# Kernel tuning notes

Hardware: AMD Instinct MI355X
Metric: run time of the kernel (lower is better)

The kernel has to match this reference:

```python
import jax, jax.numpy as jnp
import numpy as np

HIDDEN = 256
HEADS = 1
HEAD_DIM = HIDDEN // HEADS  # internal_dim == hidden (downsample_rate=1)
SQ = 4096        # 64x64 current-frame tokens
N_MEM = 4        # memory frames
N_OBJ = 64       # object-pointer tokens excluded from RoPE
SK = N_MEM * SQ + N_OBJ  # 16448


def _rotate_pairwise(x):
    # [x0, x1, x2, x3, ...] -> [-x1, x0, -x3, x2, ...]
    s = x.shape
    x = x.reshape(s[:-1] + (s[-1] // 2, 2))
    return jnp.stack([-x[..., 1], x[..., 0]], axis=-1).reshape(s)


def setup_inputs() -> dict:
    key = jax.random.key(0)
    ks = jax.random.split(key, 16)
    d = {}
    d["query"] = jax.random.normal(ks[0], (1, 1, SQ, HIDDEN), jnp.float32)
    d["key"] = jax.random.normal(ks[1], (1, 1, SK, HIDDEN), jnp.float32)
    d["value"] = jax.random.normal(ks[2], (1, 1, SK, HIDDEN), jnp.float32)
    # rotary tables broadcast over (B*P, heads) like in the keras code
    d["cos"] = jax.random.uniform(ks[3], (1, 1, SQ, HEAD_DIM), jnp.float32, -1.0, 1.0)
    d["sin"] = jax.random.uniform(ks[4], (1, 1, SQ, HEAD_DIM), jnp.float32, -1.0, 1.0)
    w = 0.02
    d["q_w"] = jax.random.normal(ks[5], (HIDDEN, HIDDEN), jnp.float32) * w
    d["q_b"] = jnp.zeros((HIDDEN,), jnp.float32)
    d["k_w"] = jax.random.normal(ks[6], (HIDDEN, HIDDEN), jnp.float32) * w
    d["k_b"] = jnp.zeros((HIDDEN,), jnp.float32)
    d["v_w"] = jax.random.normal(ks[7], (HIDDEN, HIDDEN), jnp.float32) * w
    d["v_b"] = jnp.zeros((HIDDEN,), jnp.float32)
    d["o_w"] = jax.random.normal(ks[8], (HIDDEN, HIDDEN), jnp.float32) * w
    d["o_b"] = jnp.zeros((HIDDEN,), jnp.float32)
    d["num_k_exclude_rope"] = N_OBJ
    return d


def reference(query, key, value, cos, sin, q_w, q_b, k_w, k_b, v_w, v_b, o_w, o_b, num_k_exclude_rope):
    B, P, Sq, _ = query.shape
    Sk = key.shape[2]
    nex = int(num_k_exclude_rope)

    def heads(x):  # (B,P,S,internal) -> (B*P, H, S, hd)
        s = x.shape
        return x.reshape(s[0] * s[1], s[2], HEADS, HEAD_DIM).transpose(0, 2, 1, 3)

    q = heads(query @ q_w + q_b)
    k = heads(key @ k_w + k_b)
    v = heads(value @ v_w + v_b)

    # 2D rotary embedding (fp32 math, as in the original)
    qf = q.astype(jnp.float32)
    q_emb = (qf * cos + _rotate_pairwise(qf) * sin).astype(q.dtype)

    k_rot = k[:, :, :Sk - nex, :]
    k_pass = k[:, :, Sk - nex:, :] if nex > 0 else None
    if k_rot.shape[2] != Sq:  # rope_k_repeat=True path
        rf = k_rot.shape[2] // Sq
        cos_k = jnp.repeat(cos, rf, axis=2)
        sin_k = jnp.repeat(sin, rf, axis=2)
    else:
        cos_k, sin_k = cos, sin
    kf = k_rot.astype(jnp.float32)
    k_emb = (kf * cos_k + _rotate_pairwise(kf) * sin_k).astype(k.dtype)
    if k_pass is not None:
        k_emb = jnp.concatenate([k_emb, k_pass], axis=2)

    scaling = HEAD_DIM ** -0.5
    scores = jnp.einsum('bhqd,bhkd->bhqk', q_emb, k_emb) * scaling
    attn = jax.nn.softmax(scores, axis=-1)
    out = jnp.einsum('bhqk,bhkd->bhqd', attn, v)  # (B*P, H, Sq, hd)
    out = out.transpose(0, 2, 1, 3).reshape(B, P, Sq, HEADS * HEAD_DIM)
    return out @ o_w + o_b
```

## Files before the change

kernel.cpp:

```cpp
#include <hip/hip_runtime.h>
#include <stdint.h>

typedef _Float16 half_t;
typedef __attribute__((ext_vector_type(8))) _Float16 f16x8;
typedef __attribute__((ext_vector_type(4))) _Float16 f16x4;
typedef __attribute__((ext_vector_type(4))) float f32x4;

#define SQN 4096
#define SKN 16448
#define NROPE 16384
#define NSPLIT 8
#define NTILES 514
#define TPC 65


__global__ __launch_bounds__(256) void wt_kernel(const float* __restrict__ qw,
    const float* __restrict__ kw, const float* __restrict__ vw, const float* __restrict__ ow,
    half_t* __restrict__ wt)
{
    __shared__ float tile[64][65];
    int b = blockIdx.x;
    int mat = b >> 4, t4 = b & 15;
    int k0 = (t4 >> 2) << 6, n0 = (t4 & 3) << 6;
    const float* W = (mat == 0) ? qw : (mat == 1) ? kw : (mat == 2) ? vw : ow;
    half_t* WT = wt + mat * 65536;
    int t = threadIdx.x;
#pragma unroll
    for (int j = 0; j < 16; ++j) {
        int e = j * 256 + t;
        tile[e >> 6][e & 63] = W[(k0 + (e >> 6)) * 256 + n0 + (e & 63)];
    }
    __syncthreads();
#pragma unroll
    for (int j = 0; j < 16; ++j) {
        int e = j * 256 + t;
        WT[(n0 + (e >> 6)) * 256 + k0 + (e & 63)] = (half_t)tile[e & 63][e >> 6];
    }
}

__global__ __launch_bounds__(256) void proj_kernel(
    const float* __restrict__ query, const float* __restrict__ key, const float* __restrict__ value,
    const float* __restrict__ cosp, const float* __restrict__ sinp,
    const half_t* __restrict__ wt,
    const float* __restrict__ qb, const float* __restrict__ kb, const float* __restrict__ vb,
    half_t* __restrict__ Qe, half_t* __restrict__ Ke, half_t* __restrict__ VT)
{
    __shared__ __align__(16) half_t Ws[256 * 40];
    int b = blockIdx.x;
    int mode; long row0;
    const float* X; const half_t* W; const float* bias;
    if (b < 64)       { mode = 0; row0 = (long)b * 64;         X = query; W = wt;           bias = qb; }
    else if (b < 321) { mode = 1; row0 = (long)(b - 64) * 64;  X = key;   W = wt + 65536;   bias = kb; }
    else              { mode = 2; row0 = (long)(b - 321) * 64; X = value; W = wt + 131072;  bias = vb; }

    int tid = threadIdx.x;
    int w = tid >> 6, l = tid & 63;
    int l16 = l & 15, l4 = l >> 4;
    long rw0 = row0 + w * 16;

    f32x4 acc[16];
#pragma unroll
    for (int i = 0; i < 16; ++i) acc[i] = (f32x4){0.f, 0.f, 0.f, 0.f};

    for (int ks = 0; ks < 8; ++ks) {
        __syncthreads();
        {
            const f16x8* src = reinterpret_cast<const f16x8*>(W + tid * 256 + ks * 32);
            f16x8* dst = reinterpret_cast<f16x8*>(Ws + tid * 40);
            dst[0] = src[0]; dst[1] = src[1]; dst[2] = src[2]; dst[3] = src[3];
        }
        __syncthreads();
        const float* xp = X + (rw0 + l16) * 256 + ks * 32 + l4 * 8;
        f32x4 xa = *reinterpret_cast<const f32x4*>(xp);
        f32x4 xb = *reinterpret_cast<const f32x4*>(xp + 4);
        f16x8 af;
#pragma unroll
        for (int j = 0; j < 4; ++j) { af[j] = (half_t)xa[j]; af[4 + j] = (half_t)xb[j]; }
#pragma unroll
        for (int nt = 0; nt < 16; ++nt) {
            f16x8 bf = *reinterpret_cast<const f16x8*>(Ws + (nt * 16 + l16) * 40 + l4 * 8);
            acc[nt] = __builtin_amdgcn_mfma_f32_16x16x32_f16(af, bf, acc[nt], 0, 0, 0);
        }
    }

    bool dorope = (mode == 0) || (mode == 1 && row0 < NROPE);
#pragma unroll
    for (int nt = 0; nt < 16; ++nt) {
        int d = nt * 16 + l16;
        float bv = bias[d];
        f32x4 v = acc[nt];
#pragma unroll
        for (int r = 0; r < 4; ++r) v[r] += bv;
        if (dorope) {
#pragma unroll
            for (int r = 0; r < 4; ++r) {
                long m = rw0 + l4 * 4 + r;
                long crow = (mode == 0) ? m : (m >> 2);
                float c = cosp[crow * 256 + d];
                float s = sinp[crow * 256 + d];
                float val = v[r];
                float other = __shfl_xor(val, 1);
                float rot = (d & 1) ? other : -other;
                v[r] = val * c + rot * s;
            }
        }
        if (mode == 2) {
            f16x4 pk;
#pragma unroll
            for (int r = 0; r < 4; ++r) pk[r] = (half_t)v[r];
            *reinterpret_cast<f16x4*>(VT + (long)d * SKN + rw0 + l4 * 4) = pk;
        } else {
            half_t* O = (mode == 0) ? Qe : Ke;
#pragma unroll
            for (int r = 0; r < 4; ++r)
                O[(rw0 + l4 * 4 + r) * 256 + d] = (half_t)v[r];
        }
    }
}

__global__ __launch_bounds__(512) void flash_kernel(
    const half_t* __restrict__ Qe, const half_t* __restrict__ Ke, const half_t* __restrict__ VT,
    float* __restrict__ Op, float* __restrict__ Mp, float* __restrict__ Lp)
{
    __shared__ __align__(16) half_t Ks[32 * 264];
    __shared__ __align__(16) half_t Vs[256 * 40];
    __shared__ __align__(16) half_t Ps[8][16 * 40];

    int b = blockIdx.x;
    int qb = b & 31;
    int chunk = b >> 5;
    int tid = threadIdx.x;
    int w = tid >> 6, l = tid & 63;
    int l16 = l & 15, l4 = l >> 4;
    long qw0 = (long)qb * 128 + w * 16;

    f16x8 qf[8];
#pragma unroll
    for (int ks = 0; ks < 8; ++ks)
        qf[ks] = *reinterpret_cast<const f16x8*>(Qe + (qw0 + l16) * 256 + ks * 32 + l4 * 8);

    f32x4 o[16];
#pragma unroll
    for (int i = 0; i < 16; ++i) o[i] = (f32x4){0.f, 0.f, 0.f, 0.f};
    float mrun = -3.0e38f;
    float lsum = 0.0f;

    int t0 = chunk * TPC;
    int t1 = t0 + TPC; if (t1 > NTILES) t1 = NTILES;
    const float SC = 0.090168441360f;
    half_t* Pw = Ps[w];

    for (int t = t0; t < t1; ++t) {
        long kv0 = (long)t * 32;
        __syncthreads();
        {
            int r = tid >> 4, seg = tid & 15;
            const f16x8* src = reinterpret_cast<const f16x8*>(Ke + (kv0 + r) * 256 + seg * 16);
            f16x8* dst = reinterpret_cast<f16x8*>(Ks + r * 264 + seg * 16);
            dst[0] = src[0]; dst[1] = src[1];
        }
        {
            int d = tid >> 1, seg = tid & 1;
            const f16x8* src = reinterpret_cast<const f16x8*>(VT + (long)d * SKN + kv0 + seg * 16);
            f16x8* dst = reinterpret_cast<f16x8*>(Vs + d * 40 + seg * 16);
            dst[0] = src[0]; dst[1] = src[1];
        }
        __syncthreads();

        f32x4 s0 = (f32x4){0.f, 0.f, 0.f, 0.f};
        f32x4 s1 = (f32x4){0.f, 0.f, 0.f, 0.f};
#pragma unroll
        for (int ks = 0; ks < 8; ++ks) {
            f16x8 ka0 = *reinterpret_cast<const f16x8*>(Ks + l16 * 264 + ks * 32 + l4 * 8);
            f16x8 ka1 = *reinterpret_cast<const f16x8*>(Ks + (16 + l16) * 264 + ks * 32 + l4 * 8);
            s0 = __builtin_amdgcn_mfma_f32_16x16x32_f16(ka0, qf[ks], s0, 0, 0, 0);
            s1 = __builtin_amdgcn_mfma_f32_16x16x32_f16(ka1, qf[ks], s1, 0, 0, 0);
        }

        float tv[8];
#pragma unroll
        for (int r = 0; r < 4; ++r) { tv[r] = s0[r] * SC; tv[4 + r] = s1[r] * SC; }
        float pm = tv[0];
#pragma unroll
        for (int i = 1; i < 8; ++i) pm = fmaxf(pm, tv[i]);
        pm = fmaxf(pm, __shfl_xor(pm, 16));
        pm = fmaxf(pm, __shfl_xor(pm, 32));

        if (!__all(pm - mrun <= 8.0f)) {
            float mn = fmaxf(mrun, pm);
            float alpha = __builtin_amdgcn_exp2f(mrun - mn);
            lsum *= alpha;
            float ao[4];
#pragma unroll
            for (int r = 0; r < 4; ++r) ao[r] = __shfl(alpha, l4 * 4 + r);
#pragma unroll
            for (int i = 0; i < 16; ++i)
#pragma unroll
                for (int r = 0; r < 4; ++r) o[i][r] *= ao[r];
            mrun = mn;
        }

        float p[8];
        float psum = 0.f;
#pragma unroll
        for (int i = 0; i < 8; ++i) { p[i] = __builtin_amdgcn_exp2f(tv[i] - mrun); psum += p[i]; }
        psum += __shfl_xor(psum, 16);
        psum += __shfl_xor(psum, 32);
        lsum += psum;

        f16x4 pk0, pk1;
#pragma unroll
        for (int r = 0; r < 4; ++r) { pk0[r] = (half_t)p[r]; pk1[r] = (half_t)p[4 + r]; }
        *reinterpret_cast<f16x4*>(Pw + l16 * 40 + l4 * 4) = pk0;
        *reinterpret_cast<f16x4*>(Pw + l16 * 40 + 16 + l4 * 4) = pk1;

        f16x8 pa = *reinterpret_cast<const f16x8*>(Pw + l16 * 40 + l4 * 8);
#pragma unroll
        for (int nt = 0; nt < 16; ++nt) {
            f16x8 vbf = *reinterpret_cast<const f16x8*>(Vs + (nt * 16 + l16) * 40 + l4 * 8);
            o[nt] = __builtin_amdgcn_mfma_f32_16x16x32_f16(pa, vbf, o[nt], 0, 0, 0);
        }
    }

    float* Ob = Op + ((long)chunk * SQN + qw0) * 256;
#pragma unroll
    for (int nt = 0; nt < 16; ++nt)
#pragma unroll
        for (int r = 0; r < 4; ++r)
            Ob[(l4 * 4 + r) * 256 + nt * 16 + l16] = o[nt][r];
    if (l < 16) {
        Mp[(long)chunk * SQN + qw0 + l16] = mrun;
        Lp[(long)chunk * SQN + qw0 + l16] = lsum;
    }
}

__global__ __launch_bounds__(256) void reduce_kernel(
    const float* __restrict__ Op, const float* __restrict__ Mp, const float* __restrict__ Lp,
    half_t* __restrict__ AO)
{
    int tid = threadIdx.x;
    long q = (long)blockIdx.x * 4 + (tid >> 6);
    int d0 = (tid & 63) * 4;
    float mi[NSPLIT];
    float mstar = -3.0e38f;
#pragma unroll
    for (int i = 0; i < NSPLIT; ++i) { mi[i] = Mp[i * SQN + q]; mstar = fmaxf(mstar, mi[i]); }
    f32x4 acc = (f32x4){0.f, 0.f, 0.f, 0.f};
    float lsum = 0.f;
#pragma unroll
    for (int i = 0; i < NSPLIT; ++i) {
        float wgt = __builtin_amdgcn_exp2f(mi[i] - mstar);
        lsum += wgt * Lp[i * SQN + q];
        f32x4 ov = *reinterpret_cast<const f32x4*>(Op + ((long)i * SQN + q) * 256 + d0);
#pragma unroll
        for (int r = 0; r < 4; ++r) acc[r] += wgt * ov[r];
    }
    float inv = 1.0f / lsum;
    f16x4 pk;
#pragma unroll
    for (int r = 0; r < 4; ++r) pk[r] = (half_t)(acc[r] * inv);
    *reinterpret_cast<f16x4*>(AO + q * 256 + d0) = pk;
}

__global__ __launch_bounds__(256) void oproj_kernel(
    const half_t* __restrict__ AO, const half_t* __restrict__ WTo,
    const float* __restrict__ ob, float* __restrict__ out)
{
    int b = blockIdx.x;
    int tid = threadIdx.x;
    int w = tid >> 6, l = tid & 63;
    int l16 = l & 15, l4 = l >> 4;
    long r0 = (long)b * 64 + w * 16;
    f32x4 acc[16];
#pragma unroll
    for (int i = 0; i < 16; ++i) acc[i] = (f32x4){0.f, 0.f, 0.f, 0.f};
#pragma unroll
    for (int ks = 0; ks < 8; ++ks) {
        f16x8 af = *reinterpret_cast<const f16x8*>(AO + (r0 + l16) * 256 + ks * 32 + l4 * 8);
#pragma unroll
        for (int nt = 0; nt < 16; ++nt) {
            f16x8 bf = *reinterpret_cast<const f16x8*>(WTo + (nt * 16 + l16) * 256 + ks * 32 + l4 * 8);
            acc[nt] = __builtin_amdgcn_mfma_f32_16x16x32_f16(af, bf, acc[nt], 0, 0, 0);
        }
    }
#pragma unroll
    for (int nt = 0; nt < 16; ++nt) {
        int d = nt * 16 + l16;
        float bv = ob[d];
#pragma unroll
        for (int r = 0; r < 4; ++r)
            out[(r0 + l4 * 4 + r) * 256 + d] = acc[nt][r] + bv;
    }
}

extern "C" void kernel_launch(void* const* d_in, const int* in_sizes, int n_in,
                              void* d_out, int out_size, void* d_ws, size_t ws_size,
                              hipStream_t stream) {
    const float* query = (const float*)d_in[0];
    const float* key   = (const float*)d_in[1];
    const float* value = (const float*)d_in[2];
    const float* cosp  = (const float*)d_in[3];
    const float* sinp  = (const float*)d_in[4];
    const float* qw = (const float*)d_in[5];
    const float* qb = (const float*)d_in[6];
    const float* kw = (const float*)d_in[7];
    const float* kb = (const float*)d_in[8];
    const float* vw = (const float*)d_in[9];
    const float* vb = (const float*)d_in[10];
    const float* ow = (const float*)d_in[11];
    const float* ob = (const float*)d_in[12];

    char* ws = (char*)d_ws;
    half_t* Qe = (half_t*)(ws);
    half_t* Ke = (half_t*)(ws + 2097152);
    half_t* VT = (half_t*)(ws + 10518528);
    half_t* WT = (half_t*)(ws + 18939904);
    float*  Op = (float*)(ws + 19464192);
    float*  Mp = (float*)(ws + 53018624);
    float*  Lp = (float*)(ws + 53149696);
    half_t* AO = (half_t*)(ws + 53280768);

    hipLaunchKernelGGL(wt_kernel, dim3(64), dim3(256), 0, stream, qw, kw, vw, ow, WT);
    hipLaunchKernelGGL(proj_kernel, dim3(578), dim3(256), 0, stream,
                       query, key, value, cosp, sinp, WT, qb, kb, vb, Qe, Ke, VT);
    hipLaunchKernelGGL(flash_kernel, dim3(256), dim3(512), 0, stream, Qe, Ke, VT, Op, Mp, Lp);
    hipLaunchKernelGGL(reduce_kernel, dim3(1024), dim3(256), 0, stream, Op, Mp, Lp, AO);
    hipLaunchKernelGGL(oproj_kernel, dim3(64), dim3(256), 0, stream, AO, WT + 3 * 65536, ob, (float*)d_out);
}
```

Before: 216.6 us.

## Prefetch K/V tiles, double split count, store normalized fp16 partials with LSE

The flash kernel now loads the next K/V tile into registers while computing on the current tile in LDS. This hides global latency behind the MFMA work. The split-K count doubles from 8 to 16 so more workgroups fill the GPU. Each split writes a normalized fp16 partial output plus a log2-sum-exp value instead of fp32 accumulators with separate max and sum, which halves partial traffic. The softmax scale is folded into Q during projection, and the projection kernel reads weights directly from global memory instead of staging them through LDS. Costs: extra register pressure, an fp16 rounding of partials, and a larger reduce input from more splits.

```diff
diff --git a/kernel.cpp b/kernel.cpp
--- a/kernel.cpp
+++ b/kernel.cpp
@@ -9,10 +9,9 @@
 #define SQN 4096
 #define SKN 16448
 #define NROPE 16384
-#define NSPLIT 8
+#define NSPLIT 16
 #define NTILES 514
-#define TPC 65
-
+#define SCQ 0.090168441360f
 
 __global__ __launch_bounds__(256) void wt_kernel(const float* __restrict__ qw,
     const float* __restrict__ kw, const float* __restrict__ vw, const float* __restrict__ ow,
@@ -45,7 +44,6 @@
     const float* __restrict__ qb, const float* __restrict__ kb, const float* __restrict__ vb,
     half_t* __restrict__ Qe, half_t* __restrict__ Ke, half_t* __restrict__ VT)
 {
-    __shared__ __align__(16) half_t Ws[256 * 40];
     int b = blockIdx.x;
     int mode; long row0;
     const float* X; const half_t* W; const float* bias;
@@ -62,23 +60,16 @@
 #pragma unroll
     for (int i = 0; i < 16; ++i) acc[i] = (f32x4){0.f, 0.f, 0.f, 0.f};
 
+    const float* xrow = X + (rw0 + l16) * 256;
     for (int ks = 0; ks < 8; ++ks) {
-        __syncthreads();
-        {
-            const f16x8* src = reinterpret_cast<const f16x8*>(W + tid * 256 + ks * 32);
-            f16x8* dst = reinterpret_cast<f16x8*>(Ws + tid * 40);
-            dst[0] = src[0]; dst[1] = src[1]; dst[2] = src[2]; dst[3] = src[3];
-        }
-        __syncthreads();
-        const float* xp = X + (rw0 + l16) * 256 + ks * 32 + l4 * 8;
-        f32x4 xa = *reinterpret_cast<const f32x4*>(xp);
-        f32x4 xb = *reinterpret_cast<const f32x4*>(xp + 4);
+        f32x4 xa = *reinterpret_cast<const f32x4*>(xrow + ks * 32 + l4 * 8);
+        f32x4 xb = *reinterpret_cast<const f32x4*>(xrow + ks * 32 + l4 * 8 + 4);
         f16x8 af;
 #pragma unroll
         for (int j = 0; j < 4; ++j) { af[j] = (half_t)xa[j]; af[4 + j] = (half_t)xb[j]; }
 #pragma unroll
         for (int nt = 0; nt < 16; ++nt) {
-            f16x8 bf = *reinterpret_cast<const f16x8*>(Ws + (nt * 16 + l16) * 40 + l4 * 8);
+            f16x8 bf = *reinterpret_cast<const f16x8*>(W + (nt * 16 + l16) * 256 + ks * 32 + l4 * 8);
             acc[nt] = __builtin_amdgcn_mfma_f32_16x16x32_f16(af, bf, acc[nt], 0, 0, 0);
         }
     }
@@ -102,6 +93,7 @@
                 float other = __shfl_xor(val, 1);
                 float rot = (d & 1) ? other : -other;
                 v[r] = val * c + rot * s;
+                if (mode == 0) v[r] *= SCQ;
             }
         }
         if (mode == 2) {
@@ -118,9 +110,9 @@
     }
 }
 
-__global__ __launch_bounds__(512) void flash_kernel(
+__global__ __launch_bounds__(512, 4) void flash_kernel(
     const half_t* __restrict__ Qe, const half_t* __restrict__ Ke, const half_t* __restrict__ VT,
-    float* __restrict__ Op, float* __restrict__ Mp, float* __restrict__ Lp)
+    half_t* __restrict__ AOp, float* __restrict__ Lse)
 {
     __shared__ __align__(16) half_t Ks[32 * 264];
     __shared__ __align__(16) half_t Vs[256 * 40];
@@ -134,6 +126,9 @@
     int l16 = l & 15, l4 = l >> 4;
     long qw0 = (long)qb * 128 + w * 16;
 
+    int t0 = (NTILES * chunk) / NSPLIT;
+    int t1 = (NTILES * (chunk + 1)) / NSPLIT;
+
     f16x8 qf[8];
 #pragma unroll
     for (int ks = 0; ks < 8; ++ks)
@@ -145,27 +140,31 @@
     float mrun = -3.0e38f;
     float lsum = 0.0f;
 
-    int t0 = chunk * TPC;
-    int t1 = t0 + TPC; if (t1 > NTILES) t1 = NTILES;
-    const float SC = 0.090168441360f;
+    const int krow = tid >> 4, kseg = tid & 15;
+    const int vd = tid >> 1, vseg = tid & 1;
+    f16x8* dK = reinterpret_cast<f16x8*>(Ks + krow * 264 + kseg * 16);
+    f16x8* dV = reinterpret_cast<f16x8*>(Vs + vd * 40 + vseg * 16);
+    f16x8 kr0, kr1, vr0, vr1;
+    {
+        long kv0 = (long)t0 * 32;
+        const f16x8* sK = reinterpret_cast<const f16x8*>(Ke + (kv0 + krow) * 256 + kseg * 16);
+        kr0 = sK[0]; kr1 = sK[1];
+        const f16x8* sV = reinterpret_cast<const f16x8*>(VT + (long)vd * SKN + kv0 + vseg * 16);
+        vr0 = sV[0]; vr1 = sV[1];
+    }
+    dK[0] = kr0; dK[1] = kr1; dV[0] = vr0; dV[1] = vr1;
+    __syncthreads();
+
     half_t* Pw = Ps[w];
 
     for (int t = t0; t < t1; ++t) {
-        long kv0 = (long)t * 32;
-        __syncthreads();
-        {
-            int r = tid >> 4, seg = tid & 15;
-            const f16x8* src = reinterpret_cast<const f16x8*>(Ke + (kv0 + r) * 256 + seg * 16);
-            f16x8* dst = reinterpret_cast<f16x8*>(Ks + r * 264 + seg * 16);
-            dst[0] = src[0]; dst[1] = src[1];
-        }
-        {
-            int d = tid >> 1, seg = tid & 1;
-            const f16x8* src = reinterpret_cast<const f16x8*>(VT + (long)d * SKN + kv0 + seg * 16);
-            f16x8* dst = reinterpret_cast<f16x8*>(Vs + d * 40 + seg * 16);
-            dst[0] = src[0]; dst[1] = src[1];
-        }
-        __syncthreads();
+        if (t + 1 < t1) {
+            long kv0 = (long)(t + 1) * 32;
+            const f16x8* sK = reinterpret_cast<const f16x8*>(Ke + (kv0 + krow) * 256 + kseg * 16);
+            kr0 = sK[0]; kr1 = sK[1];
+            const f16x8* sV = reinterpret_cast<const f16x8*>(VT + (long)vd * SKN + kv0 + vseg * 16);
+            vr0 = sV[0]; vr1 = sV[1];
+        }
 
         f32x4 s0 = (f32x4){0.f, 0.f, 0.f, 0.f};
         f32x4 s1 = (f32x4){0.f, 0.f, 0.f, 0.f};
@@ -179,7 +178,7 @@
 
         float tv[8];
 #pragma unroll
-        for (int r = 0; r < 4; ++r) { tv[r] = s0[r] * SC; tv[4 + r] = s1[r] * SC; }
+        for (int r = 0; r < 4; ++r) { tv[r] = s0[r]; tv[4 + r] = s1[r]; }
         float pm = tv[0];
 #pragma unroll
         for (int i = 1; i < 8; ++i) pm = fmaxf(pm, tv[i]);
@@ -220,42 +219,46 @@
             f16x8 vbf = *reinterpret_cast<const f16x8*>(Vs + (nt * 16 + l16) * 40 + l4 * 8);
             o[nt] = __builtin_amdgcn_mfma_f32_16x16x32_f16(pa, vbf, o[nt], 0, 0, 0);
         }
-    }
-
-    float* Ob = Op + ((long)chunk * SQN + qw0) * 256;
+
+        __syncthreads();
+        if (t + 1 < t1) { dK[0] = kr0; dK[1] = kr1; dV[0] = vr0; dV[1] = vr1; }
+        __syncthreads();
+    }
+
+    float inv[4];
+#pragma unroll
+    for (int r = 0; r < 4; ++r) inv[r] = 1.0f / __shfl(lsum, l4 * 4 + r);
+    half_t* Ab = AOp + ((long)chunk * SQN + qw0) * 256;
 #pragma unroll
     for (int nt = 0; nt < 16; ++nt)
 #pragma unroll
         for (int r = 0; r < 4; ++r)
-            Ob[(l4 * 4 + r) * 256 + nt * 16 + l16] = o[nt][r];
-    if (l < 16) {
-        Mp[(long)chunk * SQN + qw0 + l16] = mrun;
-        Lp[(long)chunk * SQN + qw0 + l16] = lsum;
-    }
+            Ab[(l4 * 4 + r) * 256 + nt * 16 + l16] = (half_t)(o[nt][r] * inv[r]);
+    if (l < 16)
+        Lse[(long)chunk * SQN + qw0 + l16] = mrun + __builtin_amdgcn_logf(lsum);
 }
 
 __global__ __launch_bounds__(256) void reduce_kernel(
-    const float* __restrict__ Op, const float* __restrict__ Mp, const float* __restrict__ Lp,
-    half_t* __restrict__ AO)
+    const half_t* __restrict__ AOp, const float* __restrict__ Lse, half_t* __restrict__ AO)
 {
     int tid = threadIdx.x;
     long q = (long)blockIdx.x * 4 + (tid >> 6);
     int d0 = (tid & 63) * 4;
-    float mi[NSPLIT];
-    float mstar = -3.0e38f;
-#pragma unroll
-    for (int i = 0; i < NSPLIT; ++i) { mi[i] = Mp[i * SQN + q]; mstar = fmaxf(mstar, mi[i]); }
+    float ls[NSPLIT];
+    float lmax = -3.0e38f;
+#pragma unroll
+    for (int i = 0; i < NSPLIT; ++i) { ls[i] = Lse[(long)i * SQN + q]; lmax = fmaxf(lmax, ls[i]); }
     f32x4 acc = (f32x4){0.f, 0.f, 0.f, 0.f};
-    float lsum = 0.f;
+    float wsum = 0.f;
 #pragma unroll
     for (int i = 0; i < NSPLIT; ++i) {
-        float wgt = __builtin_amdgcn_exp2f(mi[i] - mstar);
-        lsum += wgt * Lp[i * SQN + q];
-        f32x4 ov = *reinterpret_cast<const f32x4*>(Op + ((long)i * SQN + q) * 256 + d0);
-#pragma unroll
-        for (int r = 0; r < 4; ++r) acc[r] += wgt * ov[r];
-    }
-    float inv = 1.0f / lsum;
+        float wgt = __builtin_amdgcn_exp2f(ls[i] - lmax);
+        wsum += wgt;
+        f16x4 ov = *reinterpret_cast<const f16x4*>(AOp + ((long)i * SQN + q) * 256 + d0);
+#pragma unroll
+        for (int r = 0; r < 4; ++r) acc[r] += wgt * (float)ov[r];
+    }
+    float inv = 1.0f / wsum;
     f16x4 pk;
 #pragma unroll
     for (int r = 0; r < 4; ++r) pk[r] = (half_t)(acc[r] * inv);
@@ -311,19 +314,18 @@
     const float* ob = (const float*)d_in[12];
 
     char* ws = (char*)d_ws;
-    half_t* Qe = (half_t*)(ws);
-    half_t* Ke = (half_t*)(ws + 2097152);
-    half_t* VT = (half_t*)(ws + 10518528);
-    half_t* WT = (half_t*)(ws + 18939904);
-    float*  Op = (float*)(ws + 19464192);
-    float*  Mp = (float*)(ws + 53018624);
-    float*  Lp = (float*)(ws + 53149696);
-    half_t* AO = (half_t*)(ws + 53280768);
+    half_t* Qe  = (half_t*)(ws);
+    half_t* Ke  = (half_t*)(ws + 2097152);
+    half_t* VT  = (half_t*)(ws + 10518528);
+    half_t* WT  = (half_t*)(ws + 18939904);
+    half_t* AOp = (half_t*)(ws + 19464192);
+    float*  Lse = (float*)(ws + 53018624);
+    half_t* AO  = (half_t*)(ws + 53280768);
 
     hipLaunchKernelGGL(wt_kernel, dim3(64), dim3(256), 0, stream, qw, kw, vw, ow, WT);
     hipLaunchKernelGGL(proj_kernel, dim3(578), dim3(256), 0, stream,
                        query, key, value, cosp, sinp, WT, qb, kb, vb, Qe, Ke, VT);
-    hipLaunchKernelGGL(flash_kernel, dim3(256), dim3(512), 0, stream, Qe, Ke, VT, Op, Mp, Lp);
-    hipLaunchKernelGGL(reduce_kernel, dim3(1024), dim3(256), 0, stream, Op, Mp, Lp, AO);
+    hipLaunchKernelGGL(flash_kernel, dim3(32 * NSPLIT), dim3(512), 0, stream, Qe, Ke, VT, AOp, Lse);
+    hipLaunchKernelGGL(reduce_kernel, dim3(1024), dim3(256), 0, stream, AOp, Lse, AO);
     hipLaunchKernelGGL(oproj_kernel, dim3(64), dim3(256), 0, stream, AO, WT + 3 * 65536, ob, (float*)d_out);
 }
```

New measurement: 348.4 us. 60.8% more time.
